# Optimization experiments

Hardware: AMD Instinct MI355X
Metric: run time of the kernel (lower is better)

Reference implementation:

```python
import jax, jax.numpy as jnp
import numpy as np

EPS = 1e-7

def squash(s, axis=-1):
    # s * ||s||^2 / (1 + ||s||^2) / ||s||
    sq_norm = jnp.sum(jnp.square(s), axis=axis, keepdims=True)
    scale = sq_norm / (1.0 + sq_norm) / jnp.sqrt(sq_norm + EPS)
    return scale * s

def setup_inputs() -> dict:
    key = jax.random.key(0)
    k1, k2 = jax.random.split(key)
    B, I, K = 64, 2048, 16   # batch, input_num_capsule, input_dim_capsule
    N, D = 32, 32            # num_capsule, dim_capsule
    inputs = jax.random.normal(k1, (B, I, K), dtype=jnp.float32)
    W = jax.random.normal(k2, (N, I, D, K), dtype=jnp.float32) * 0.05
    return {"inputs": inputs, "W": W}

def reference(inputs, W, routings=3):
    # u_hat[b,n,i,d] = sum_k inputs[b,i,k] * W[n,i,d,k]
    # (tile over n + per-sample batch_dot in the original, fused here)
    u_hat = jnp.einsum('bik,nidk->bnid', inputs, W)  # [B,N,I,D]
    B, N, I, D = u_hat.shape
    b = jnp.zeros((B, N, I), dtype=u_hat.dtype)
    outputs = None
    for r in range(routings):
        c = jax.nn.softmax(b, axis=1)                          # softmax over num_capsule
        s = jnp.einsum('bni,bnid->bnd', c, u_hat)              # weighted sum over input caps
        outputs = squash(s)                                    # [B,N,D]
        if r < routings - 1:
            b = b + jnp.einsum('bnd,bnid->bni', outputs, u_hat)  # agreement update
    return outputs
```

## Files before the change

kernel.cpp:

```cpp
#include <hip/hip_runtime.h>
#include <hip/hip_bf16.h>
#include <math.h>

#define B_ 64
#define I_ 2048
#define K_ 16
#define N_ 32
#define D_ 32
#define SCH_ 16

#define AS1 __attribute__((address_space(1)))
#define AS3 __attribute__((address_space(3)))

typedef __attribute__((ext_vector_type(8))) short short8_t;
typedef __attribute__((ext_vector_type(4))) float f32x4_t;

#define OFF_INT   0u
#define OFF_CT    2097152u
#define OFF_BT    6291456u
#define OFF_SPART 10485760u
#define OFF_OFRAG 11534336u
#define OFF_XFRAG 11599872u
#define OFF_WFS   12648448u
#define OFF_WFU   29425664u

__device__ __forceinline__ unsigned int pk_bf16(float lo, float hi) {
    union { __hip_bfloat162 h2; unsigned int u; } cv;
    cv.h2 = __float22bfloat162_rn(float2{lo, hi});
    return cv.u;
}

__global__ __launch_bounds__(256) void k_prep(const float* __restrict__ in,
                                              float* __restrict__ inT,
                                              uint4* __restrict__ xfrag) {
    __shared__ float lds[B_][K_ + 1];
    const int i = blockIdx.x;
    const int t = threadIdx.x;
    const int b = t >> 2, kq = t & 3;
    const float4 v = *(const float4*)(in + ((size_t)b * I_ + i) * K_ + kq * 4);
    lds[b][kq * 4 + 0] = v.x; lds[b][kq * 4 + 1] = v.y;
    lds[b][kq * 4 + 2] = v.z; lds[b][kq * 4 + 3] = v.w;
    __syncthreads();
#pragma unroll
    for (int q = 0; q < 4; ++q) {
        const int j = t + q * 256;
        const int k = j >> 6, bb = j & 63;
        inT[(size_t)i * (K_ * B_) + j] = lds[bb][k];
    }
    if (t < 128) {
        const int m = t >> 5, r = t & 31, gl = r >> 4, kl = r & 15;
        const int bb = m * 16 + kl, k0 = 8 * gl;
        union { unsigned int u[4]; uint4 q; } o;
#pragma unroll
        for (int p = 0; p < 4; ++p)
            o.u[p] = pk_bf16(lds[bb][k0 + 2 * p], lds[bb][k0 + 2 * p + 1]);
        xfrag[((size_t)m * 1024 + (i >> 1)) * 64 + (2 * (i & 1) + gl) * 16 + kl] = o.q;
    }
}

__global__ __launch_bounds__(512, 4) void k_wpack(const float* __restrict__ W,
                                                  uint4* __restrict__ wfs,
                                                  uint4* __restrict__ wfu) {
    __shared__ __align__(16) float lds[2048];
    const int ib = blockIdx.x * 16;
    const int n = blockIdx.y;
    const int t = threadIdx.x, w = t >> 6, lane = t & 63;
    const float* wg = W + ((size_t)n * I_ + ib) * 512;

    for (int sc = 0; sc < 4; ++sc) {
        __syncthreads();
        {
            const float4* s4 = (const float4*)(wg + sc * 2048);
            float4* d4 = (float4*)lds;
            __builtin_amdgcn_global_load_lds(
                (const AS1 void*)(const void*)(s4 + w * 64 + lane),
                (AS3 void*)(void*)(d4 + w * 64), 16, 0, 0);
        }
        __syncthreads();

        if (t < 256) {
            const int il = t >> 6, l = t & 63, g = l >> 4, kl = l & 15;
            const float* base = lds + il * 512;
            union { unsigned int u[4]; uint4 q; } o;
#pragma unroll
            for (int p = 0; p < 4; ++p)
                o.u[p] = pk_bf16(base[(8 * g + 2 * p) * 16 + kl],
                                 base[(8 * g + 2 * p + 1) * 16 + kl]);
            wfu[((size_t)n * I_ + ib + sc * 4 + il) * 64 + l] = o.q;
        } else {
            const int u2 = t - 256;
            const int kkl = u2 >> 7, r = u2 & 127, nt = r >> 6, l = r & 63, g = l >> 4;
            const float* p = lds + kkl * 1024 + (g >> 1) * 512 + nt * 256
                             + (l & 15) * 16 + (g & 1) * 8;
            const float4 f0 = *(const float4*)p;
            const float4 f1 = *(const float4*)(p + 4);
            union { unsigned int u[4]; uint4 q; } o;
            o.u[0] = pk_bf16(f0.x, f0.y); o.u[1] = pk_bf16(f0.z, f0.w);
            o.u[2] = pk_bf16(f1.x, f1.y); o.u[3] = pk_bf16(f1.z, f1.w);
            const int kk = (ib >> 1) + sc * 2 + kkl;
            wfs[(((size_t)n * 1024 + kk) * 2 + nt) * 64 + l] = o.q;
        }
    }
}

template<int UNIFORM>
__global__ __launch_bounds__(512, 2) void k_sweep_mfma(const uint4* __restrict__ wfs,
                                                       const uint4* __restrict__ xfrag,
                                                       const float* __restrict__ cT,
                                                       float* __restrict__ spart) {
    __shared__ float red[2][B_][D_ + 1];
    const int n = blockIdx.y, ch = blockIdx.x;
    const int t = threadIdx.x, w = t >> 6, l = t & 63;
    const int m = w >> 1, ks = w & 1;

    f32x4_t acc0 = {0.f, 0.f, 0.f, 0.f};
    f32x4_t acc1 = {0.f, 0.f, 0.f, 0.f};

    const uint4* xf = xfrag + (size_t)m * 65536 + l;
    const uint4* wf = wfs + (size_t)n * (1024 * 128) + l;
    const int kk0 = ch * 64 + ks * 32;

    for (int tt = 0; tt < 32; ++tt) {
        const int kk = kk0 + tt;
        union { uint4 q; unsigned int u[4]; } xv;
        xv.q = xf[(size_t)kk * 64];
        union { unsigned int u[4]; short8_t v; } af;
        if (UNIFORM) {
            af.u[0] = xv.u[0]; af.u[1] = xv.u[1];
            af.u[2] = xv.u[2]; af.u[3] = xv.u[3];
        } else {
            const float c = cT[((size_t)n * I_ + 2 * kk + (l >> 5)) * B_
                               + m * 16 + (l & 15)];
#pragma unroll
            for (int p = 0; p < 4; ++p) {
                const unsigned int uu = xv.u[p];
                const float lo = __uint_as_float(uu << 16);
                const float hi = __uint_as_float(uu & 0xffff0000u);
                af.u[p] = pk_bf16(lo * c, hi * c);
            }
        }
        union { uint4 q; short8_t v; } b0, b1;
        b0.q = wf[(size_t)kk * 128];
        b1.q = wf[(size_t)kk * 128 + 64];

        acc0 = __builtin_amdgcn_mfma_f32_16x16x32_bf16(af.v, b0.v, acc0, 0, 0, 0);
        acc1 = __builtin_amdgcn_mfma_f32_16x16x32_bf16(af.v, b1.v, acc1, 0, 0, 0);
    }

#pragma unroll
    for (int r = 0; r < 4; ++r) {
        const int row = m * 16 + (l >> 4) * 4 + r;
        red[ks][row][(l & 15)]      = acc0[r];
        red[ks][row][16 + (l & 15)] = acc1[r];
    }
    __syncthreads();
#pragma unroll
    for (int q = 0; q < 4; ++q) {
        const int j = q * 512 + t;
        const int b = j >> 5, d = j & 31;
        spart[((size_t)n * SCH_ + ch) * (B_ * D_) + j] = red[0][b][d] + red[1][b][d];
    }
}

template<int FINAL>
__global__ __launch_bounds__(256) void k_reduce(const float* __restrict__ spart,
                                                unsigned int* __restrict__ ofrag_u32,
                                                float* __restrict__ out,
                                                float prescale) {
    const int gt = blockIdx.x * 256 + threadIdx.x;
    const int n = gt >> 11;
    const int rem = gt & 2047;
    const int b = rem >> 5, d = rem & 31;
    const float* sp = spart + (size_t)n * (SCH_ * B_ * D_) + rem;
    float s = 0.f;
#pragma unroll
    for (int p = 0; p < SCH_; ++p) s += sp[p * (B_ * D_)];
    s *= prescale;

    float sq = s * s;
#pragma unroll
    for (int off = 16; off >= 1; off >>= 1) sq += __shfl_xor(sq, off, 64);
    const float scale = sq / ((1.0f + sq) * sqrtf(sq + 1e-7f));
    const float o = scale * s;
    if (FINAL) {
        out[((size_t)b * N_ + n) * D_ + d] = o;
    } else {
        const float o_next = __shfl_down(o, 1, 64);
        if ((d & 1) == 0) {
            const unsigned int val = pk_bf16(o, o_next);
            const int l = (d >> 3) * 16 + (b & 15);
            ofrag_u32[(((n * 4 + (b >> 4)) * 64) + l) * 4 + ((d & 7) >> 1)] = val;
        }
    }
}

template<int FIRST>
__global__ __launch_bounds__(512, 2) void k_updsm(const uint4* __restrict__ wfu,
                                                  const float* __restrict__ inT,
                                                  const uint4* __restrict__ ofrag,
                                                  float* __restrict__ bT,
                                                  float* __restrict__ cT) {
    const int t = threadIdx.x, w = t >> 6, l = t & 63;
    const int btile = w & 3;
    const int i = blockIdx.x * 2 + (w >> 2);
    const int g = l >> 4, kl = l & 15;
    const int bp = btile * 16 + kl;

    float x4[4];
    {
        const float* xp = inT + (size_t)i * (K_ * B_) + bp;
#pragma unroll
        for (int r = 0; r < 4; ++r) x4[r] = xp[(4 * g + r) * B_];
    }

    float bn[N_];
#pragma unroll
    for (int n = 0; n < N_; ++n) {
        union { uint4 q; short8_t v; } of, af;
        of.q = ofrag[(n * 4 + btile) * 64 + l];
        af.q = wfu[((size_t)n * I_ + i) * 64 + l];
        f32x4_t acc = {0.f, 0.f, 0.f, 0.f};
        acc = __builtin_amdgcn_mfma_f32_16x16x32_bf16(af.v, of.v, acc, 0, 0, 0);
        float gp = 0.f;
#pragma unroll
        for (int r = 0; r < 4; ++r) gp = fmaf(acc[r], x4[r], gp);
        gp += __shfl_xor(gp, 16, 64);
        gp += __shfl_xor(gp, 32, 64);
        const size_t bi = ((size_t)n * I_ + i) * B_ + bp;
        if (FIRST) {
            if (l < 16) bT[bi] = gp;
        } else {
            gp += bT[bi];
        }
        bn[n] = gp;
    }

    float mx = bn[0];
#pragma unroll
    for (int n = 1; n < N_; ++n) mx = fmaxf(mx, bn[n]);
    float sum = 0.f;
#pragma unroll
    for (int n = 0; n < N_; ++n) { bn[n] = __expf(bn[n] - mx); sum += bn[n]; }
    const float inv = 1.0f / sum;
    if (l < 16) {
#pragma unroll
        for (int n = 0; n < N_; ++n)
            cT[((size_t)n * I_ + i) * B_ + bp] = bn[n] * inv;
    }
}

extern "C" void kernel_launch(void* const* d_in, const int* in_sizes, int n_in,
                              void* d_out, int out_size, void* d_ws, size_t ws_size,
                              hipStream_t stream) {
    const float* inputs = (const float*)d_in[0];
    const float* W      = (const float*)d_in[1];
    float* out = (float*)d_out;
    float* ws  = (float*)d_ws;
    float* inT   = ws + OFF_INT;
    float* cT    = ws + OFF_CT;
    float* bT    = ws + OFF_BT;
    float* spart = ws + OFF_SPART;
    unsigned int* ofrag_u32 = (unsigned int*)(ws + OFF_OFRAG);
    uint4* ofrag = (uint4*)(ws + OFF_OFRAG);
    uint4* xfrag = (uint4*)(ws + OFF_XFRAG);
    uint4* wfs   = (uint4*)(ws + OFF_WFS);
    uint4* wfu   = (uint4*)(ws + OFF_WFU);

    k_wpack<<<dim3(I_ / 16, N_), 512, 0, stream>>>(W, wfs, wfu);
    k_prep<<<I_, 256, 0, stream>>>(inputs, inT, xfrag);
    k_sweep_mfma<1><<<dim3(SCH_, N_), 512, 0, stream>>>(wfs, xfrag, cT, spart);
    k_reduce<0><<<256, 256, 0, stream>>>(spart, ofrag_u32, out, 1.0f / N_);
    k_updsm<1><<<I_ / 2, 512, 0, stream>>>(wfu, inT, ofrag, bT, cT);
    k_sweep_mfma<0><<<dim3(SCH_, N_), 512, 0, stream>>>(wfs, xfrag, cT, spart);
    k_reduce<0><<<256, 256, 0, stream>>>(spart, ofrag_u32, out, 1.0f);
    k_updsm<0><<<I_ / 2, 512, 0, stream>>>(wfu, inT, ofrag, bT, cT);
    k_sweep_mfma<0><<<dim3(SCH_, N_), 512, 0, stream>>>(wfs, xfrag, cT, spart);
    k_reduce<1><<<256, 256, 0, stream>>>(spart, ofrag_u32, out, 1.0f);
}
```

Baseline: 180.5 us.

## Load whole W tile into LDS at once with XOR-swizzled layout in k_wpack

The weight packing kernel now issues all four global-to-LDS chunk loads up front into a 32KB LDS buffer with one barrier, instead of alternating load/sync/process four times. The global source addresses are XOR-swizzled so the LDS layout avoids bank conflicts on the strided reads, and the reads apply the matching swizzle through helper functions. This removes per-chunk barrier stalls and exposes more memory parallelism. The cost is four times the LDS per block, which may reduce occupancy under the 4-block launch bound.

Result: faster. 176.7 us (-2.1%).

```diff
diff --git a/kernel.cpp b/kernel.cpp
--- a/kernel.cpp
+++ b/kernel.cpp
@@ -28,6 +28,17 @@
     union { __hip_bfloat162 h2; unsigned int u; } cv;
     cv.h2 = __float22bfloat162_rn(float2{lo, hi});
     return cv.u;
+}
+
+__device__ __forceinline__ float lds_rd(const float* lds, int A) {
+    const int G = A >> 2;
+    const int S = G ^ ((G >> 5) & 7);
+    return lds[(S << 2) | (A & 3)];
+}
+__device__ __forceinline__ float4 lds_rd4(const float* lds, int A) {
+    const int G = A >> 2;
+    const int S = G ^ ((G >> 5) & 7);
+    return *(const float4*)(lds + (S << 2));
 }
 
 __global__ __launch_bounds__(256) void k_prep(const float* __restrict__ in,
@@ -61,39 +72,44 @@
 __global__ __launch_bounds__(512, 4) void k_wpack(const float* __restrict__ W,
                                                   uint4* __restrict__ wfs,
                                                   uint4* __restrict__ wfu) {
-    __shared__ __align__(16) float lds[2048];
+    __shared__ __align__(16) float lds[8192];
     const int ib = blockIdx.x * 16;
     const int n = blockIdx.y;
-    const int t = threadIdx.x, w = t >> 6, lane = t & 63;
-    const float* wg = W + ((size_t)n * I_ + ib) * 512;
-
+    const int t = threadIdx.x, w = t >> 6;
+    const float4* wg4 = (const float4*)(W + ((size_t)n * I_ + ib) * 512);
+
+#pragma unroll
     for (int sc = 0; sc < 4; ++sc) {
-        __syncthreads();
-        {
-            const float4* s4 = (const float4*)(wg + sc * 2048);
-            float4* d4 = (float4*)lds;
-            __builtin_amdgcn_global_load_lds(
-                (const AS1 void*)(const void*)(s4 + w * 64 + lane),
-                (AS3 void*)(void*)(d4 + w * 64), 16, 0, 0);
-        }
-        __syncthreads();
-
-        if (t < 256) {
-            const int il = t >> 6, l = t & 63, g = l >> 4, kl = l & 15;
-            const float* base = lds + il * 512;
+        const int S = sc * 512 + t;
+        const int gg = S ^ ((S >> 5) & 7);
+        __builtin_amdgcn_global_load_lds(
+            (const AS1 void*)(const void*)(wg4 + gg),
+            (AS3 void*)(void*)((float4*)lds + sc * 512 + w * 64), 16, 0, 0);
+    }
+    __syncthreads();
+
+    if (t < 256) {
+        const int il = t >> 6, l = t & 63, g = l >> 4, kl = l & 15;
+#pragma unroll
+        for (int sc = 0; sc < 4; ++sc) {
+            const int base = (sc * 4 + il) * 512;
             union { unsigned int u[4]; uint4 q; } o;
 #pragma unroll
             for (int p = 0; p < 4; ++p)
-                o.u[p] = pk_bf16(base[(8 * g + 2 * p) * 16 + kl],
-                                 base[(8 * g + 2 * p + 1) * 16 + kl]);
+                o.u[p] = pk_bf16(lds_rd(lds, base + (8 * g + 2 * p) * 16 + kl),
+                                 lds_rd(lds, base + (8 * g + 2 * p + 1) * 16 + kl));
             wfu[((size_t)n * I_ + ib + sc * 4 + il) * 64 + l] = o.q;
-        } else {
-            const int u2 = t - 256;
-            const int kkl = u2 >> 7, r = u2 & 127, nt = r >> 6, l = r & 63, g = l >> 4;
-            const float* p = lds + kkl * 1024 + (g >> 1) * 512 + nt * 256
-                             + (l & 15) * 16 + (g & 1) * 8;
-            const float4 f0 = *(const float4*)p;
-            const float4 f1 = *(const float4*)(p + 4);
+        }
+    } else {
+        const int u2 = t - 256;
+        const int kkl = u2 >> 7, r = u2 & 127, nt = r >> 6, l = r & 63, g = l >> 4;
+        const int Floc = kkl * 1024 + (g >> 1) * 512 + nt * 256
+                         + (l & 15) * 16 + (g & 1) * 8;
+#pragma unroll
+        for (int sc = 0; sc < 4; ++sc) {
+            const int F = sc * 2048 + Floc;
+            const float4 f0 = lds_rd4(lds, F);
+            const float4 f1 = lds_rd4(lds, F + 4);
             union { unsigned int u[4]; uint4 q; } o;
             o.u[0] = pk_bf16(f0.x, f0.y); o.u[1] = pk_bf16(f0.z, f0.w);
             o.u[2] = pk_bf16(f1.x, f1.y); o.u[3] = pk_bf16(f1.z, f1.w);
```
